# Optimization experiments

Hardware: AMD Instinct MI355X
Metric: run time of the kernel (lower is better)

The kernel has to match this reference:

```python
import jax, jax.numpy as jnp
import numpy as np

N = 8192        # agents (single node type VEHICLE)
K = 15          # max_Nnode - 1 neighbors per node
E = N * K       # edges
FT = 12         # prediction horizon steps
SD = 4          # state dim (x, y, vx, vy)
ID = 2          # input dim (ax, ay)
ZD = 8          # latent z dim
HE = 256        # history_enc_dim
EE = 128        # edge_enc_dim
OH = 256        # obs_lstm_hidden_dim
GH = 256        # guide_RNN_hidden_dim
FH = 256        # FC_hidden_dim
AD = 16         # att_internal_dim
DT = 0.25
SCALE = 1.0     # input_scale


def setup_inputs() -> dict:
    ks = jax.random.split(jax.random.key(0), 40)
    f = lambda i, s: jax.random.normal(ks[i], s, jnp.float32)
    w = lambda i, s: 0.05 * jax.random.normal(ks[i], s, jnp.float32)
    inp = dict(
        x_last=f(0, (N, SD)), x_st_last=f(1, (N, SD)), hist_enc=f(2, (N, HE)),
        z=f(3, (N, ZD)),
        node_size=jax.random.uniform(ks[4], (N, 2), jnp.float32, 1.0, 3.0),
        W_h0=w(5, (SD, OH)), b_h0=w(6, (OH,)), W_c0=w(7, (SD, OH)), b_c0=w(8, (OH,)),
        W_gh=w(9, (HE + ZD, GH)), b_gh=w(10, (GH,)),
        W_gru_ih=w(11, (HE + ZD, 3 * GH)), W_gru_hh=w(12, (GH, 3 * GH)),
        b_gru_ih=w(13, (3 * GH,)), b_gru_hh=w(14, (3 * GH,)),
        W_proj=w(15, (GH, 2)), b_proj=w(16, (2,)),
        W_att1=w(17, (EE, AD)), W_att2=w(18, (SD, AD)), v_att=w(19, (AD,)),
        W_lstm_ih=w(20, (EE, 4 * OH)), W_lstm_hh=w(21, (OH, 4 * OH)),
        b_lstm_ih=w(22, (4 * OH,)), b_lstm_hh=w(23, (4 * OH,)),
        W_e1=w(24, (SD + 4, FH)), b_e1=w(25, (FH,)), W_e2=w(26, (FH, EE)), b_e2=w(27, (EE,)),
        W_a1=w(28, (OH + ZD + SD + 4, FH)), b_a1=w(29, (FH,)),
        W_a2=w(30, (FH, ID)), b_a2=w(31, (ID,)),
    )
    # edge k is the j-th neighbor of node k // K; index 0 in the enc table is the pad row
    inp["edge_idx1"] = jnp.repeat(jnp.arange(N), K)
    inp["edge_idx2"] = jax.random.randint(ks[32], (E,), 0, N)
    inp["node_obs_idx"] = (jnp.arange(E) + 1).reshape(N, K)
    inp["ft"] = FT
    return inp


def _dyn(s, u):
    # double-integrator: s = [x, y, vx, vy], u = [ax, ay]
    pos = s[:, :2] + s[:, 2:4] * DT + 0.5 * u * DT * DT
    vel = s[:, 2:4] + u * DT
    return jnp.concatenate([pos, vel], -1)


def _forward(x_last, x_st_last, hist_enc, z, node_size,
             W_h0, b_h0, W_c0, b_c0, W_gh, b_gh, W_gru_ih, W_gru_hh, b_gru_ih, b_gru_hh,
             W_proj, b_proj, W_att1, W_att2, v_att, W_lstm_ih, W_lstm_hh, b_lstm_ih, b_lstm_hh,
             W_e1, b_e1, W_e2, b_e2, W_a1, b_a1, W_a2, b_a2,
             edge_idx1, edge_idx2, node_obs_idx, ft):
    n = x_last.shape[0]
    ee = W_e2.shape[1]
    # ---- guide GRU: desired trajectory [ft, N, 2] ----
    xz = jnp.concatenate([hist_enc, z], -1)
    h0g = xz @ W_gh + b_gh
    gi = xz @ W_gru_ih + b_gru_ih  # input is constant over time (xz repeated)
    ir, iz, inn = jnp.split(gi, 3, -1)

    def gru_step(h, _):
        hr, hz, hn = jnp.split(h @ W_gru_hh + b_gru_hh, 3, -1)
        r = jax.nn.sigmoid(ir + hr)
        u = jax.nn.sigmoid(iz + hz)
        nh = (1.0 - u) * jnp.tanh(inn + r * hn) + u * h
        return nh, nh

    _, hs = jax.lax.scan(gru_step, h0g, None, length=ft)
    des = hs @ W_proj + b_proj                       # [ft, N, 2]
    des_next = jnp.concatenate([des[1:], des[-1:]], 0)
    des_prev = jnp.concatenate([jnp.zeros_like(des[:1]), des[:-1]], 0)
    first = jnp.zeros((ft,), jnp.float32).at[0].set(1.0)

    # ---- obs LSTM initial state ----
    h0 = x_st_last @ W_h0 + b_h0
    c0 = x_st_last @ W_c0 + b_c0

    size1 = node_size[edge_idx1]
    size2 = node_size[edge_idx2]
    rad = 0.5 * (jnp.linalg.norm(size1, axis=-1) + jnp.linalg.norm(size2, axis=-1))

    def step(carry, xs):
        prev, prev_st, h, c, terr, ccost = carry
        des_t, des_n, des_p, fst = xs
        # edge gather + collision cost + edge encoding
        s1 = prev[edge_idx1]
        s2 = prev[edge_idx2]
        dist = jnp.linalg.norm(s1[:, :2] - s2[:, :2], axis=-1)
        ccost = ccost + jnp.sum(jax.nn.relu(rad - dist))
        feat = jnp.concatenate([s2 - s1, size1, size2], -1)          # [E, SD+4]
        enc = jax.nn.relu(feat @ W_e1 + b_e1) @ W_e2 + b_e2          # [E, EE]
        enc_all = jnp.concatenate([jnp.zeros((1, ee), enc.dtype), enc], 0)
        obs = enc_all[node_obs_idx]                                   # [N, K, EE]
        # relative state (t==0 uses standardized history directly)
        m = 1.0 - fst
        rel = prev_st - m * x_st_last
        rel = jnp.concatenate([rel[:, :2] - m * des_p, rel[:, 2:]], -1)
        terr = terr + jnp.linalg.norm(rel[:, :2]) / n
        next_wp = des_t - prev_st[:, :2]
        next_wp2 = des_n - prev_st[:, :2]
        # additive attention over neighbors
        scores = jnp.tanh(obs @ W_att1 + (rel @ W_att2)[:, None, :]) @ v_att   # [N, K]
        att = jax.nn.softmax(scores, axis=-1)
        ctx = jnp.einsum('nk,nkd->nd', att, obs)
        # LSTM cell (torch gate order i, f, g, o)
        gates = ctx @ W_lstm_ih + b_lstm_ih + h @ W_lstm_hh + b_lstm_hh
        g_i, g_f, g_g, g_o = jnp.split(gates, 4, -1)
        c = jax.nn.sigmoid(g_f) * c + jax.nn.sigmoid(g_i) * jnp.tanh(g_g)
        h = jax.nn.sigmoid(g_o) * jnp.tanh(c)
        # action net + dynamics rollout
        a_in = jnp.concatenate([h, z, rel, next_wp, next_wp2], -1)   # [N, OH+ZD+SD+4]
        u = SCALE * jnp.tanh(jax.nn.relu(a_in @ W_a1 + b_a1) @ W_a2 + b_a2)
        nxt = _dyn(prev, u)
        nxt_st = _dyn(prev_st, u)
        return (nxt, nxt_st, h, c, terr, ccost), (nxt, u)

    zero = jnp.zeros((), jnp.float32)
    init = (x_last, x_st_last, h0, c0, zero, zero)
    (_, _, _, _, terr, ccost), (state_pred, input_pred) = jax.lax.scan(
        step, init, (des, des_next, des_prev, first))
    return state_pred, input_pred, terr, ccost


def reference(x_last, x_st_last, hist_enc, z, node_size,
              W_h0, b_h0, W_c0, b_c0, W_gh, b_gh, W_gru_ih, W_gru_hh, b_gru_ih, b_gru_hh,
              W_proj, b_proj, W_att1, W_att2, v_att, W_lstm_ih, W_lstm_hh, b_lstm_ih, b_lstm_hh,
              W_e1, b_e1, W_e2, b_e2, W_a1, b_a1, W_a2, b_a2,
              edge_idx1, edge_idx2, node_obs_idx, ft):
    return _forward(x_last, x_st_last, hist_enc, z, node_size,
                    W_h0, b_h0, W_c0, b_c0, W_gh, b_gh, W_gru_ih, W_gru_hh, b_gru_ih, b_gru_hh,
                    W_proj, b_proj, W_att1, W_att2, v_att, W_lstm_ih, W_lstm_hh, b_lstm_ih, b_lstm_hh,
                    W_e1, b_e1, W_e2, b_e2, W_a1, b_a1, W_a2, b_a2,
                    edge_idx1, edge_idx2, node_obs_idx, ft)
```

## Files before the change

### kernel.cpp

```cpp
#include <hip/hip_runtime.h>

#define DEVI __device__ __forceinline__

constexpr int N_  = 8192;
constexpr int K_  = 15;
constexpr int E_  = N_ * K_;
constexpr int FTS = 12;
constexpr float DT_ = 0.25f;

typedef __attribute__((ext_vector_type(8))) short short8x;
typedef __attribute__((ext_vector_type(4))) float float4x;

union U8 { unsigned int u[4]; short8x v; };

DEVI float sigf(float x) { return 1.0f / (1.0f + __expf(-x)); }
DEVI float tanhf_fast(float x) { float e = __expf(2.f * x); return 1.f - 2.f / (e + 1.f); }
DEVI unsigned int f2u(float x) { union { float f; unsigned int u; } c; c.f = x; return c.u; }
DEVI float u2f(unsigned int x) { union { unsigned int u; float f; } c; c.u = x; return c.f; }

DEVI void split8(const float* __restrict__ s, short8x& hi8, short8x& lo8) {
  U8 ph, pl;
#pragma unroll
  for (int p = 0; p < 4; p++) {
    float a0 = s[2*p], a1 = s[2*p+1];
    unsigned int u0 = f2u(a0), u1 = f2u(a1);
    unsigned int h0 = u0 & 0xFFFF0000u, h1 = u1 & 0xFFFF0000u;
    ph.u[p] = (u0 >> 16) | h1;
    float l0 = a0 - u2f(h0), l1 = a1 - u2f(h1);
    pl.u[p] = (f2u(l0) >> 16) | (f2u(l1) & 0xFFFF0000u);
  }
  hi8 = ph.v; lo8 = pl.v;
}

__global__ void k_zero(float* ss) {
  ss[blockIdx.x * 256 + threadIdx.x] = 0.f;
}

__global__ __launch_bounds__(256) void k_init_des(const float* __restrict__ b_proj,
                                                  float* __restrict__ des) {
  int i = blockIdx.x * 256 + threadIdx.x;
  des[i*2]     = b_proj[0];
  des[i*2 + 1] = b_proj[1];
}

__global__ __launch_bounds__(256) void k_edge_static(
    const int* __restrict__ e1, const int* __restrict__ e2,
    const float* __restrict__ nsize, float* __restrict__ rad, float* __restrict__ szf)
{
  int e = blockIdx.x * 256 + threadIdx.x;
  if (e >= E_) return;
  int i1 = e1[e], i2 = e2[e];
  float s1x = nsize[i1*2+0], s1y = nsize[i1*2+1];
  float s2x = nsize[i2*2+0], s2y = nsize[i2*2+1];
  rad[e] = 0.5f * (sqrtf(s1x*s1x + s1y*s1y) + sqrtf(s2x*s2x + s2y*s2y));
  *(float4*)&szf[e*4] = make_float4(s1x, s1y, s2x, s2y);
}

__global__ __launch_bounds__(256) void k_prep_hi(
    const float* __restrict__ W, unsigned short* __restrict__ out)
{
  int t = blockIdx.x * 256 + threadIdx.x;
  int fid = t >> 6, L = t & 63;
  int ks = fid >> 3, nt = fid & 7;
  int k0 = ks * 32 + (L >> 4) * 8;
  int n  = nt * 16 + (L & 15);
  unsigned int hi[4];
#pragma unroll
  for (int p = 0; p < 4; p++) {
    float w0 = W[(size_t)(k0 + 2*p) * 128 + n];
    float w1 = W[(size_t)(k0 + 2*p + 1) * 128 + n];
    hi[p] = (f2u(w0) >> 16) | (f2u(w1) & 0xFFFF0000u);
  }
  *(uint4*)(out + (size_t)fid * 512 + (size_t)L * 8) = make_uint4(hi[0], hi[1], hi[2], hi[3]);
}

__global__ __launch_bounds__(256) void k_prep1(
    const float* __restrict__ WA, const float* __restrict__ WB,
    int mode, int split, int wA, int wB, int Ktot, int NT, int nfrag,
    unsigned short* __restrict__ out)
{
  int t = blockIdx.x * 256 + threadIdx.x;
  int fid = t >> 6, L = t & 63;
  if (fid >= nfrag) return;
  int ks = fid / NT, nt = fid % NT;
  int k0 = ks * 32 + (L >> 4) * 8;
  int n  = nt * 16 + (L & 15);
  unsigned int hi[4];
#pragma unroll
  for (int p = 0; p < 4; p++) {
    float w0 = 0.f, w1 = 0.f;
    int ka = k0 + 2*p, kb = ka + 1;
    if (mode == 0) {
      if (ka < Ktot) w0 = (ka < split) ? WA[(size_t)ka*wA + n] : WB[(size_t)(ka-split)*wB + n];
      if (kb < Ktot) w1 = (kb < split) ? WA[(size_t)kb*wA + n] : WB[(size_t)(kb-split)*wB + n];
    } else {
      if (ka < Ktot) w0 = (n < split) ? WA[(size_t)ka*wA + n] : WB[(size_t)ka*wB + (n-split)];
      if (kb < Ktot) w1 = (n < split) ? WA[(size_t)kb*wA + n] : WB[(size_t)kb*wB + (n-split)];
    }
    hi[p] = (f2u(w0) >> 16) | (f2u(w1) & 0xFFFF0000u);
  }
  *(uint4*)(out + (size_t)fid * 512 + (size_t)L * 8) = make_uint4(hi[0], hi[1], hi[2], hi[3]);
}

__global__ __launch_bounds__(256) void k_xz_mfma(
    const float* __restrict__ hist, const float* __restrict__ z,
    const unsigned short* __restrict__ wB,
    const float* __restrict__ b_gh, const float* __restrict__ b_gih,
    float* __restrict__ gh0, float* __restrict__ gi)
{
  __shared__ __align__(16) float Abuf[2][64][36];
  const int tid = threadIdx.x;
  const int w = tid >> 6, lane = tid & 63;
  const int m = lane & 15, q = lane >> 4;
  const int n0 = blockIdx.x * 64;
  const int r_ = tid >> 2, c_ = (tid & 3) * 8;
  float4x acc[16];
#pragma unroll
  for (int tl = 0; tl < 16; tl++) acc[tl] = (float4x){0.f,0.f,0.f,0.f};

  auto LD = [&](int ks, float4& v0, float4& v1) {
    int kk = ks*32 + c_;
    int n = n0 + r_;
    if (kk < 256) {
      v0 = *(const float4*)&hist[(size_t)n*256 + kk];
      v1 = *(const float4*)&hist[(size_t)n*256 + kk + 4];
    } else if (kk == 256) {
      v0 = *(const float4*)&z[n*8];
      v1 = *(const float4*)&z[n*8 + 4];
    } else {
      v0 = make_float4(0,0,0,0); v1 = v0;
    }
  };
  {
    float4 v0, v1; LD(0, v0, v1);
    *(float4*)&Abuf[0][r_][c_]     = v0;
    *(float4*)&Abuf[0][r_][c_ + 4] = v1;
  }
  __syncthreads();
  for (int ks = 0; ks < 9; ks++) {
    float4 v0, v1;
    if (ks < 8) LD(ks + 1, v0, v1);
    short8x aHi, aLo;
    split8(&Abuf[ks & 1][w*16 + m][q*8], aHi, aLo);
#pragma unroll
    for (int tl = 0; tl < 16; tl++) {
      int nt = blockIdx.y*16 + tl;
      size_t off = (size_t)(ks*64 + nt) * 512 + (size_t)lane*8;
      short8x bh = *(const short8x*)(wB + off);
      acc[tl] = __builtin_amdgcn_mfma_f32_16x16x32_bf16(aLo, bh, acc[tl], 0, 0, 0);
      acc[tl] = __builtin_amdgcn_mfma_f32_16x16x32_bf16(aHi, bh, acc[tl], 0, 0, 0);
    }
    if (ks < 8) {
      *(float4*)&Abuf[(ks+1) & 1][r_][c_]     = v0;
      *(float4*)&Abuf[(ks+1) & 1][r_][c_ + 4] = v1;
      __syncthreads();
    }
  }
#pragma unroll
  for (int tl = 0; tl < 16; tl++) {
    int col = (blockIdx.y*16 + tl)*16 + m;
    float bias = (col < 256) ? b_gh[col] : b_gih[col - 256];
#pragma unroll
    for (int i = 0; i < 4; i++) {
      int n = n0 + w*16 + q*4 + i;
      float v = acc[tl][i] + bias;
      if (col < 256) gh0[(size_t)n*256 + col] = v;
      else           gi[(size_t)n*768 + col - 256] = v;
    }
  }
}

DEVI void gru_core(float* sm, int tid, int n0, int j0,
                   const float* __restrict__ h_in, const unsigned short* __restrict__ wB,
                   const float* __restrict__ b_hh, const float* __restrict__ gi,
                   const float* __restrict__ W_proj, float* __restrict__ des_t,
                   float* __restrict__ h_out)
{
  float (*A0)[36] = (float (*)[36])sm;
  float (*A1)[36] = (float (*)[36])(sm + 2304);
  const int w = tid >> 6, lane = tid & 63;
  const int m = lane & 15, q = lane >> 4;
  const int r_ = tid >> 2, c_ = (tid & 3) * 8;
  float4x acc[12];
#pragma unroll
  for (int tl = 0; tl < 12; tl++) acc[tl] = (float4x){0.f,0.f,0.f,0.f};

  {
    float4 p0 = *(const float4*)&h_in[(size_t)(n0 + r_)*256 + c_];
    float4 p1 = *(const float4*)&h_in[(size_t)(n0 + r_)*256 + c_ + 4];
    *(float4*)&A0[r_][c_]     = p0;
    *(float4*)&A0[r_][c_ + 4] = p1;
  }
  __syncthreads();
  for (int ks = 0; ks < 8; ks++) {
    float4 p0, p1;
    if (ks < 7) {
      int kk = (ks + 1)*32 + c_;
      p0 = *(const float4*)&h_in[(size_t)(n0 + r_)*256 + kk];
      p1 = *(const float4*)&h_in[(size_t)(n0 + r_)*256 + kk + 4];
    }
    float (*Ac)[36] = (ks & 1) ? A1 : A0;
    short8x aHi, aLo;
    split8(&Ac[w*16 + m][q*8], aHi, aLo);
#pragma unroll
    for (int tl = 0; tl < 12; tl++) {
      int g = tl >> 2, jt = tl & 3;
      int nt = g*16 + (j0 >> 4) + jt;
      size_t off = (size_t)(ks*48 + nt) * 512 + (size_t)lane*8;
      short8x bh = *(const short8x*)(wB + off);
      acc[tl] = __builtin_amdgcn_mfma_f32_16x16x32_bf16(aLo, bh, acc[tl], 0, 0, 0);
      acc[tl] = __builtin_amdgcn_mfma_f32_16x16x32_bf16(aHi, bh, acc[tl], 0, 0, 0);
    }
    if (ks < 7) {
      float (*An)[36] = (ks & 1) ? A0 : A1;
      *(float4*)&An[r_][c_]     = p0;
      *(float4*)&An[r_][c_ + 4] = p1;
      __syncthreads();
    }
  }
  float pd0[4] = {0,0,0,0}, pd1[4] = {0,0,0,0};
#pragma unroll
  for (int jt = 0; jt < 4; jt++) {
    int j = j0 + jt*16 + m;
    float br = b_hh[j], bz = b_hh[256 + j], bn = b_hh[512 + j];
    float wp0 = W_proj[j*2], wp1 = W_proj[j*2 + 1];
#pragma unroll
    for (int i = 0; i < 4; i++) {
      int n = n0 + w*16 + q*4 + i;
      float ir  = gi[(size_t)n*768 + j];
      float iz  = gi[(size_t)n*768 + 256 + j];
      float inn = gi[(size_t)n*768 + 512 + j];
      float hold = h_in[(size_t)n*256 + j];
      float r = sigf(ir + acc[0*4 + jt][i] + br);
      float u = sigf(iz + acc[1*4 + jt][i] + bz);
      float nh = (1.f - u) * tanhf_fast(inn + r * (acc[2*4 + jt][i] + bn)) + u * hold;
      h_out[(size_t)n*256 + j] = nh;
      pd0[i] += nh * wp0;
      pd1[i] += nh * wp1;
    }
  }
#pragma unroll
  for (int off = 1; off < 16; off <<= 1) {
#pragma unroll
    for (int i = 0; i < 4; i++) {
      pd0[i] += __shfl_xor(pd0[i], off);
      pd1[i] += __shfl_xor(pd1[i], off);
    }
  }
  if (m == 0) {
#pragma unroll
    for (int i = 0; i < 4; i++) {
      int n = n0 + w*16 + q*4 + i;
      atomicAdd(&des_t[n*2],     pd0[i]);
      atomicAdd(&des_t[n*2 + 1], pd1[i]);
    }
  }
}

__global__ __launch_bounds__(256) void k_gru_mfma(
    const float* __restrict__ h_in, const unsigned short* __restrict__ wB,
    const float* __restrict__ b_hh, const float* __restrict__ gi,
    const float* __restrict__ W_proj, float* __restrict__ des_t,
    float* __restrict__ h_out)
{
  __shared__ __align__(16) float smem[4608];
  gru_core(smem, threadIdx.x, blockIdx.x * 64, blockIdx.y * 64,
           h_in, wB, b_hh, gi, W_proj, des_t, h_out);
}

__global__ __launch_bounds__(256) void k_lstm_mfma(
    const float* __restrict__ ctxg, const float* __restrict__ h_in,
    const unsigned short* __restrict__ wB,
    const float* __restrict__ b_ih, const float* __restrict__ b_hh,
    float* __restrict__ c_st, float* __restrict__ h_out)
{
  __shared__ __align__(16) float Abuf[2][64][36];
  const int tid = threadIdx.x;
  const int w = tid >> 6, lane = tid & 63;
  const int m = lane & 15, q = lane >> 4;
  const int n0 = blockIdx.x * 64;
  const int j0 = blockIdx.y * 32;
  const int r_ = tid >> 2, c_ = (tid & 3) * 8;
  float4x acc[8];
#pragma unroll
  for (int tl = 0; tl < 8; tl++) acc[tl] = (float4x){0.f,0.f,0.f,0.f};

  auto LD = [&](int ks, float4& v0, float4& v1) {
    int kk = ks*32 + c_;
    int n = n0 + r_;
    if (kk < 128) {
      v0 = *(const float4*)&ctxg[(size_t)n*128 + kk];
      v1 = *(const float4*)&ctxg[(size_t)n*128 + kk + 4];
    } else {
      v0 = *(const float4*)&h_in[(size_t)n*256 + kk - 128];
      v1 = *(const float4*)&h_in[(size_t)n*256 + kk - 124];
    }
  };
  {
    float4 v0, v1; LD(0, v0, v1);
    *(float4*)&Abuf[0][r_][c_]     = v0;
    *(float4*)&Abuf[0][r_][c_ + 4] = v1;
  }
  __syncthreads();
  for (int ks = 0; ks < 12; ks++) {
    float4 v0, v1;
    if (ks < 11) LD(ks + 1, v0, v1);
    short8x aHi, aLo;
    split8(&Abuf[ks & 1][w*16 + m][q*8], aHi, aLo);
#pragma unroll
    for (int tl = 0; tl < 8; tl++) {
      int g = tl >> 1, jt = tl & 1;
      int nt = g*16 + (j0 >> 4) + jt;
      size_t off = (size_t)(ks*64 + nt) * 512 + (size_t)lane*8;
      short8x bh = *(const short8x*)(wB + off);
      acc[tl] = __builtin_amdgcn_mfma_f32_16x16x32_bf16(aLo, bh, acc[tl], 0, 0, 0);
      acc[tl] = __builtin_amdgcn_mfma_f32_16x16x32_bf16(aHi, bh, acc[tl], 0, 0, 0);
    }
    if (ks < 11) {
      *(float4*)&Abuf[(ks+1) & 1][r_][c_]     = v0;
      *(float4*)&Abuf[(ks+1) & 1][r_][c_ + 4] = v1;
      __syncthreads();
    }
  }
#pragma unroll
  for (int jt = 0; jt < 2; jt++) {
    int j = j0 + jt*16 + m;
    float bi = b_ih[j]       + b_hh[j];
    float bf = b_ih[256 + j] + b_hh[256 + j];
    float bg = b_ih[512 + j] + b_hh[512 + j];
    float bo = b_ih[768 + j] + b_hh[768 + j];
#pragma unroll
    for (int i = 0; i < 4; i++) {
      int n = n0 + w*16 + q*4 + i;
      float g_i = sigf(acc[0*2 + jt][i] + bi);
      float g_f = sigf(acc[1*2 + jt][i] + bf);
      float g_g = tanhf_fast(acc[2*2 + jt][i] + bg);
      float g_o = sigf(acc[3*2 + jt][i] + bo);
      float cv = g_f * c_st[(size_t)n*256 + j] + g_i * g_g;
      c_st[(size_t)n*256 + j] = cv;
      h_out[(size_t)n*256 + j] = g_o * tanhf_fast(cv);
    }
  }
}

__global__ __launch_bounds__(256) void k_action_mfma(
    const float* __restrict__ h, const float* __restrict__ z,
    const float* __restrict__ rel, const float* __restrict__ nwp, const float* __restrict__ nwp2,
    const unsigned short* __restrict__ wB, const float* __restrict__ b_a1,
    const float* __restrict__ W_a2, const float* __restrict__ b_a2,
    float* __restrict__ prev, float* __restrict__ prev_st,
    float* __restrict__ outS, float* __restrict__ outU)
{
  __shared__ __align__(16) float Abuf[2][32][36];
  __shared__ float sm_p[2][16][2];
  const int tid = threadIdx.x;
  const int w = tid >> 6, lane = tid & 63;
  const int m = lane & 15, q = lane >> 4;
  const int ng = w >> 1, hh = w & 1;
  const int n0 = blockIdx.x * 32;
  const int r_ = tid >> 3, c_ = (tid & 7) * 4;
  float4x acc[8];
#pragma unroll
  for (int j = 0; j < 8; j++) acc[j] = (float4x){0.f,0.f,0.f,0.f};

  auto LD = [&](int ks) -> float4 {
    int kk = ks*32 + c_;
    int n = n0 + r_;
    float4 v;
    if (kk < 256)       v = *(const float4*)&h[(size_t)n*256 + kk];
    else if (kk == 256) v = *(const float4*)&z[n*8];
    else if (kk == 260) v = *(const float4*)&z[n*8 + 4];
    else if (kk == 264) v = *(const float4*)&rel[n*4];
    else if (kk == 268) {
      float2 w1 = *(const float2*)&nwp[n*2];
      float2 w2 = *(const float2*)&nwp2[n*2];
      v = make_float4(w1.x, w1.y, w2.x, w2.y);
    } else v = make_float4(0,0,0,0);
    return v;
  };
  {
    float4 v = LD(0);
    *(float4*)&Abuf[0][r_][c_] = v;
  }
  __syncthreads();
  for (int ks = 0; ks < 9; ks++) {
    float4 v;
    if (ks < 8) v = LD(ks + 1);
    short8x aHi, aLo;
    split8(&Abuf[ks & 1][ng*16 + m][q*8], aHi, aLo);
#pragma unroll
    for (int j = 0; j < 8; j++) {
      int tl = hh*8 + j;
      size_t off = (size_t)(ks*16 + tl) * 512 + (size_t)lane*8;
      short8x bh = *(const short8x*)(wB + off);
      acc[j] = __builtin_amdgcn_mfma_f32_16x16x32_bf16(aLo, bh, acc[j], 0, 0, 0);
      acc[j] = __builtin_amdgcn_mfma_f32_16x16x32_bf16(aHi, bh, acc[j], 0, 0, 0);
    }
    if (ks < 8) {
      *(float4*)&Abuf[(ks+1) & 1][r_][c_] = v;
      __syncthreads();
    }
  }
  float p0[4] = {0,0,0,0}, p1[4] = {0,0,0,0};
#pragma unroll
  for (int j = 0; j < 8; j++) {
    int col = (hh*8 + j)*16 + m;
    float ba = b_a1[col];
    float2 w2 = *(const float2*)&W_a2[col*2];
#pragma unroll
    for (int i = 0; i < 4; i++) {
      float hv = fmaxf(acc[j][i] + ba, 0.f);
      p0[i] += hv * w2.x;
      p1[i] += hv * w2.y;
    }
  }
#pragma unroll
  for (int off = 1; off < 16; off <<= 1) {
#pragma unroll
    for (int i = 0; i < 4; i++) {
      p0[i] += __shfl_xor(p0[i], off);
      p1[i] += __shfl_xor(p1[i], off);
    }
  }
  if (hh == 1 && m == 0) {
#pragma unroll
    for (int i = 0; i < 4; i++) {
      sm_p[ng][q*4 + i][0] = p0[i];
      sm_p[ng][q*4 + i][1] = p1[i];
    }
  }
  __syncthreads();
  if (hh == 0 && m == 0) {
    float ba0 = b_a2[0], ba1 = b_a2[1];
    const float hd = 0.5f * DT_ * DT_;
#pragma unroll
    for (int i = 0; i < 4; i++) {
      int n = n0 + ng*16 + q*4 + i;
      float ux = tanhf_fast(p0[i] + sm_p[ng][q*4 + i][0] + ba0);
      float uy = tanhf_fast(p1[i] + sm_p[ng][q*4 + i][1] + ba1);
      float4 pv = *(const float4*)&prev[n*4];
      float4 ps = *(const float4*)&prev_st[n*4];
      float4 npv, nps;
      npv.x = pv.x + pv.z*DT_ + ux*hd;
      npv.y = pv.y + pv.w*DT_ + uy*hd;
      npv.z = pv.z + ux*DT_;
      npv.w = pv.w + uy*DT_;
      nps.x = ps.x + ps.z*DT_ + ux*hd;
      nps.y = ps.y + ps.w*DT_ + uy*hd;
      nps.z = ps.z + ux*DT_;
      nps.w = ps.w + uy*DT_;
      *(float4*)&prev[n*4] = npv;
      *(float4*)&prev_st[n*4] = nps;
      *(float4*)&outS[(size_t)n*4] = npv;
      outU[n*2]     = ux;
      outU[n*2 + 1] = uy;
    }
  }
}

__global__ __launch_bounds__(256) void k_init_hc(
    const float* __restrict__ x_last, const float* __restrict__ x_st_last,
    const float* __restrict__ W_h0, const float* __restrict__ b_h0,
    const float* __restrict__ W_c0, const float* __restrict__ b_c0,
    float* __restrict__ h, float* __restrict__ c,
    float* __restrict__ prev, float* __restrict__ prev_st)
{
  const int n = blockIdx.x;
  const int j = threadIdx.x;
  float x0 = x_st_last[n*4], x1 = x_st_last[n*4+1], x2 = x_st_last[n*4+2], x3 = x_st_last[n*4+3];
  h[(size_t)n*256 + j] = b_h0[j] + x0*W_h0[j] + x1*W_h0[256+j] + x2*W_h0[512+j] + x3*W_h0[768+j];
  c[(size_t)n*256 + j] = b_c0[j] + x0*W_c0[j] + x1*W_c0[256+j] + x2*W_c0[512+j] + x3*W_c0[768+j];
  if (j < 4) prev[n*4 + j] = x_last[n*4 + j];
  else if (j < 8) prev_st[n*4 + (j-4)] = x_st_last[n*4 + (j-4)];
}

__global__ __launch_bounds__(256, 4) void k_edge_gru(
    const float* __restrict__ prev, const float* __restrict__ prev_st,
    const float* __restrict__ x_st_last,
    const float* __restrict__ szf, const float* __restrict__ rad,
    const int* __restrict__ nobs, const int* __restrict__ e1, const int* __restrict__ e2,
    const float* __restrict__ W_e1, const float* __restrict__ b_e1,
    const unsigned short* __restrict__ wsB, const float* __restrict__ b_e2,
    const unsigned short* __restrict__ wattA, const float* __restrict__ W_att2,
    const float* __restrict__ v_att,
    const float* __restrict__ des_p, const float* __restrict__ des_t,
    const float* __restrict__ des_n,
    float* __restrict__ relg, float* __restrict__ nwp, float* __restrict__ nwp2,
    float* __restrict__ ctx, float* __restrict__ ss_t, float* __restrict__ cc,
    const float* __restrict__ g_hin, const unsigned short* __restrict__ wBg,
    const float* __restrict__ b_ghh, const float* __restrict__ gi,
    const float* __restrict__ W_proj, float* __restrict__ des_g,
    float* __restrict__ g_hout, int gru_on)
{
  __shared__ __align__(16) float smem[4776];
  const int tid = threadIdx.x;
  const int bid = blockIdx.x;

  if ((bid % 5) == 4) {
    if (!gru_on) return;
    int b = bid / 5;
    gru_core(smem, tid, (b & 127) * 64, (b >> 7) * 64,
             g_hin, wBg, b_ghh, gi, W_proj, des_g, g_hout);
    return;
  }
  const int eb = bid - (bid + 1) / 5;

  float* sm_stage = smem;
  float* sm_feats = smem + 4096;
  float* sm_flags = smem + 4608;
  float* sm_relv  = smem + 4672;
  float* sm_watt2 = smem + 4688;
  float* sm_vatt  = smem + 4752;
  float* sm_red   = smem + 4768;

  const int n0  = eb * 4;
  const int slot = (eb & 15) << 4;
  const int lane = tid & 63;
  const int g    = tid >> 6;
  const int q = lane >> 4, m = lane & 15;

  if (tid >= 176 && tid < 192) sm_vatt[tid - 176] = v_att[tid - 176];
  if (tid >= 192) sm_watt2[tid - 192] = W_att2[tid - 192];

  if (tid < 64) {
    float v = 0.f;
    if (tid < 60) {
      int gg = tid / 15, k = tid % 15;
      int idx = nobs[(n0 + gg) * 15 + k];
      float f[8] = {0,0,0,0,0,0,0,0};
      float fl = 0.f;
      if (idx > 0) {
        int e = idx - 1;
        int i1 = e1[e], i2 = e2[e];
#pragma unroll
        for (int d = 0; d < 4; d++) f[d] = prev[i2*4 + d] - prev[i1*4 + d];
        float4 sz = *(const float4*)&szf[(size_t)e*4];
        f[4] = sz.x; f[5] = sz.y; f[6] = sz.z; f[7] = sz.w;
        fl = 1.f;
        float dist = sqrtf(f[0]*f[0] + f[1]*f[1]);
        v = fmaxf(rad[e] - dist, 0.f);
      }
#pragma unroll
      for (int d = 0; d < 8; d++) sm_feats[(gg*16 + k)*8 + d] = f[d];
      sm_flags[gg*16 + k] = fl;
    } else {
      int gg = tid - 60;
#pragma unroll
      for (int d = 0; d < 8; d++) sm_feats[(gg*16 + 15)*8 + d] = 0.f;
      sm_flags[gg*16 + 15] = 0.f;
    }
#pragma unroll
    for (int off = 32; off; off >>= 1) v += __shfl_down(v, off);
    if (tid == 0) atomicAdd(cc + slot, v);
  } else if (tid < 68) {
    int gg = tid - 64;
    int n = n0 + gg;
    float4 ps = *(const float4*)&prev_st[n*4];
    float r0, r1, r2, r3;
    if (des_p) {
      float4 xs = *(const float4*)&x_st_last[n*4];
      r0 = ps.x - xs.x - des_p[n*2];
      r1 = ps.y - xs.y - des_p[n*2 + 1];
      r2 = ps.z - xs.z;
      r3 = ps.w - xs.w;
    } else { r0 = ps.x; r1 = ps.y; r2 = ps.z; r3 = ps.w; }
    sm_relv[gg*4+0] = r0; sm_relv[gg*4+1] = r1; sm_relv[gg*4+2] = r2; sm_relv[gg*4+3] = r3;
    *(float4*)&relg[n*4] = make_float4(r0, r1, r2, r3);
    nwp[n*2]      = des_t[n*2]     - ps.x;
    nwp[n*2 + 1]  = des_t[n*2 + 1] - ps.y;
    nwp2[n*2]     = des_n[n*2]     - ps.x;
    nwp2[n*2 + 1] = des_n[n*2 + 1] - ps.y;
    sm_red[gg] = r0*r0 + r1*r1;
  }
  {
    const uint4* src = (const uint4*)wsB;
    uint4* dst = (uint4*)sm_stage;
    dst[tid]       = src[tid];
    dst[tid + 256] = src[tid + 256];
  }
  __syncthreads();
  if (tid == 64) atomicAdd(ss_t + slot, sm_red[0] + sm_red[1] + sm_red[2] + sm_red[3]);

  float f[8];
  {
    const float4 fa = *(const float4*)&sm_feats[(g*16 + m)*8];
    const float4 fb = *(const float4*)&sm_feats[(g*16 + m)*8 + 4];
    f[0]=fa.x; f[1]=fa.y; f[2]=fa.z; f[3]=fa.w; f[4]=fb.x; f[5]=fb.y; f[6]=fb.z; f[7]=fb.w;
  }
  float4x encR[8];
#pragma unroll
  for (int nt = 0; nt < 8; nt++) encR[nt] = (float4x){0.f,0.f,0.f,0.f};
  const float4* We14 = (const float4*)W_e1;
  const float4* Be14 = (const float4*)b_e1;

  for (int ks = 0; ks < 8; ks++) {
    uint4 r0, r1;
    if (ks < 7) {
      const uint4* src = (const uint4*)wsB + (ks + 1) * 512;
      r0 = src[tid];
      r1 = src[tid + 256];
    }
    short8x aHi, aLo;
    {
      float h8[8];
      float4 b0 = Be14[8*ks + 2*q];
      float4 b1 = Be14[8*ks + 2*q + 1];
      h8[0]=b0.x; h8[1]=b0.y; h8[2]=b0.z; h8[3]=b0.w; h8[4]=b1.x; h8[5]=b1.y; h8[6]=b1.z; h8[7]=b1.w;
#pragma unroll
      for (int d = 0; d < 8; d++) {
        float4 wa = We14[d*64 + ks*8 + 2*q];
        float4 wb = We14[d*64 + ks*8 + 2*q + 1];
        h8[0] += f[d]*wa.x; h8[1] += f[d]*wa.y; h8[2] += f[d]*wa.z; h8[3] += f[d]*wa.w;
        h8[4] += f[d]*wb.x; h8[5] += f[d]*wb.y; h8[6] += f[d]*wb.z; h8[7] += f[d]*wb.w;
      }
#pragma unroll
      for (int p = 0; p < 8; p++) h8[p] = fmaxf(h8[p], 0.f);
      split8(h8, aHi, aLo);
    }
    const unsigned short* sb = (const unsigned short*)sm_stage + (ks & 1) * 4096;
#pragma unroll
    for (int nt = 0; nt < 8; nt++) {
      short8x bh = *(const short8x*)(sb + nt*512 + lane*8);
      encR[nt] = __builtin_amdgcn_mfma_f32_16x16x32_bf16(aLo, bh, encR[nt], 0, 0, 0);
      encR[nt] = __builtin_amdgcn_mfma_f32_16x16x32_bf16(aHi, bh, encR[nt], 0, 0, 0);
    }
    if (ks < 7) {
      uint4* dst = (uint4*)sm_stage + ((ks + 1) & 1) * 512;
      dst[tid]       = r0;
      dst[tid + 256] = r1;
      __syncthreads();
    }
  }
  float4x fl4 = *(const float4x*)&sm_flags[g*16 + q*4];
#pragma unroll
  for (int nt = 0; nt < 8; nt++) {
    float b2 = b_e2[nt*16 + m];
#pragma unroll
    for (int i = 0; i < 4; i++) encR[nt][i] = (encR[nt][i] + b2) * fl4[i];
  }

  __syncthreads();
  {
  }
  float* tb = sm_stage + g * 576;
  float4x sacc = {0.f, 0.f, 0.f, 0.f};
#pragma unroll
  for (int ksc = 0; ksc < 4; ksc++) {
#pragma unroll
    for (int ntl = 0; ntl < 2; ntl++) {
#pragma unroll
      for (int i = 0; i < 4; i++)
        tb[(q*4 + i)*36 + ntl*16 + m] = encR[2*ksc + ntl][i];
    }
    __builtin_amdgcn_s_waitcnt(0);
    float a8[8];
    {
      const float4* tp = (const float4*)(tb + m*36 + q*8);
      float4 t0 = tp[0], t1 = tp[1];
      a8[0]=t0.x; a8[1]=t0.y; a8[2]=t0.z; a8[3]=t0.w;
      a8[4]=t1.x; a8[5]=t1.y; a8[6]=t1.z; a8[7]=t1.w;
    }
    __builtin_amdgcn_s_waitcnt(0);
    short8x aH, aL;
    split8(a8, aH, aL);
    short8x bh = *(const short8x*)(wattA + ksc*512 + lane*8);
    sacc = __builtin_amdgcn_mfma_f32_16x16x32_bf16(aL, bh, sacc, 0, 0, 0);
    sacc = __builtin_amdgcn_mfma_f32_16x16x32_bf16(aH, bh, sacc, 0, 0, 0);
  }

  float relw;
  {
    float4 rv = *(const float4*)&sm_relv[g*4];
    relw = rv.x * sm_watt2[m] + rv.y * sm_watt2[16 + m]
         + rv.z * sm_watt2[32 + m] + rv.w * sm_watt2[48 + m];
  }
  float vat = sm_vatt[m];
  float val[4];
#pragma unroll
  for (int i = 0; i < 4; i++) val[i] = tanhf_fast(sacc[i] + relw) * vat;
#pragma unroll
  for (int msk = 1; msk < 16; msk <<= 1) {
#pragma unroll
    for (int i = 0; i < 4; i++) val[i] += __shfl_xor(val[i], msk);
  }
  if (q == 3) val[3] = -3.0e38f;
  float mx = fmaxf(fmaxf(val[0], val[1]), fmaxf(val[2], val[3]));
  mx = fmaxf(mx, __shfl_xor(mx, 16));
  mx = fmaxf(mx, __shfl_xor(mx, 32));
  float4x ev;
  float ssum = 0.f;
#pragma unroll
  for (int i = 0; i < 4; i++) { ev[i] = __expf(val[i] - mx); ssum += ev[i]; }
  ssum += __shfl_xor(ssum, 16);
  ssum += __shfl_xor(ssum, 32);
  float inv = 1.f / ssum;
#pragma unroll
  for (int i = 0; i < 4; i++) ev[i] *= inv;

  float cpart[8];
#pragma unroll
  for (int nt = 0; nt < 8; nt++) {
    float cv = ev[0]*encR[nt][0] + ev[1]*encR[nt][1] + ev[2]*encR[nt][2] + ev[3]*encR[nt][3];
    cv += __shfl_xor(cv, 16);
    cv += __shfl_xor(cv, 32);
    cpart[nt] = cv;
  }
  float v0 = (q == 0) ? cpart[0] : (q == 1) ? cpart[2] : (q == 2) ? cpart[4] : cpart[6];
  float v1 = (q == 0) ? cpart[1] : (q == 1) ? cpart[3] : (q == 2) ? cpart[5] : cpart[7];
  size_t cb = (size_t)(n0 + g) * 128 + q*32 + m;
  ctx[cb]      = v0;
  ctx[cb + 16] = v1;
}

__global__ void k_final(const float* __restrict__ ss, float* __restrict__ out) {
  const int lane = threadIdx.x;
  float red[13];
#pragma unroll
  for (int a = 0; a < 13; a++) {
    float v = (lane < 16) ? ss[a*256 + lane*16] : 0.f;
    v += __shfl_xor(v, 1);
    v += __shfl_xor(v, 2);
    v += __shfl_xor(v, 4);
    v += __shfl_xor(v, 8);
    red[a] = v;
  }
  if (lane == 0) {
    float t = 0.f;
    for (int i = 0; i < FTS; i++) t += sqrtf(red[i]);
    out[(size_t)FTS * N_ * 6]     = t / (float)N_;
    out[(size_t)FTS * N_ * 6 + 1] = red[12];
  }
}

extern "C" void kernel_launch(void* const* d_in, const int* in_sizes, int n_in,
                              void* d_out, int out_size, void* d_ws, size_t ws_size,
                              hipStream_t stream) {
  (void)in_sizes; (void)n_in; (void)out_size;
  const float* x_last    = (const float*)d_in[0];
  const float* x_st_last = (const float*)d_in[1];
  const float* hist_enc  = (const float*)d_in[2];
  const float* z         = (const float*)d_in[3];
  const float* node_size = (const float*)d_in[4];
  const float* W_h0 = (const float*)d_in[5];
  const float* b_h0 = (const float*)d_in[6];
  const float* W_c0 = (const float*)d_in[7];
  const float* b_c0 = (const float*)d_in[8];
  const float* W_gh = (const float*)d_in[9];
  const float* b_gh = (const float*)d_in[10];
  const float* W_gih = (const float*)d_in[11];
  const float* W_ghh = (const float*)d_in[12];
  const float* b_gih = (const float*)d_in[13];
  const float* b_ghh = (const float*)d_in[14];
  const float* W_proj = (const float*)d_in[15];
  const float* b_proj = (const float*)d_in[16];
  const float* W_att1 = (const float*)d_in[17];
  const float* W_att2 = (const float*)d_in[18];
  const float* v_att  = (const float*)d_in[19];
  const float* W_lih = (const float*)d_in[20];
  const float* W_lhh = (const float*)d_in[21];
  const float* b_lih = (const float*)d_in[22];
  const float* b_lhh = (const float*)d_in[23];
  const float* W_e1 = (const float*)d_in[24];
  const float* b_e1 = (const float*)d_in[25];
  const float* W_e2 = (const float*)d_in[26];
  const float* b_e2 = (const float*)d_in[27];
  const float* W_a1 = (const float*)d_in[28];
  const float* b_a1 = (const float*)d_in[29];
  const float* W_a2 = (const float*)d_in[30];
  const float* b_a2 = (const float*)d_in[31];
  const int* e1   = (const int*)d_in[32];
  const int* e2   = (const int*)d_in[33];
  const int* nobs = (const int*)d_in[34];
  float* out = (float*)d_out;

  float* wsf     = (float*)d_ws;
  float* prev    = wsf;
  float* prev_st = wsf + 32768;
  float* des     = wsf + 65536;
  float* rad     = wsf + 262160;
  float* szf     = wsf + 385040;
  float* baseA   = wsf + 876560;
  float* gh0 = baseA;
  float* gh1 = baseA + (size_t)N_ * 256;
  float* gi  = baseA + (size_t)2 * N_ * 256;
  float* hA   = baseA;
  float* hB   = baseA + (size_t)N_ * 256;
  float* cbuf = baseA + (size_t)2 * N_ * 256;
  float* ctx  = baseA + (size_t)3 * N_ * 256;
  float* rel  = baseA + (size_t)4 * N_ * 256;
  float* nwp  = rel + (size_t)N_ * 4;
  float* nwp2 = nwp + (size_t)N_ * 2;
  unsigned short* wsBe = (unsigned short*)(wsf + 11362320);
  unsigned short* wsBg = (unsigned short*)(wsf + 11427856);
  unsigned short* wsBl = (unsigned short*)(wsf + 11624464);
  unsigned short* wsBx = (unsigned short*)(wsf + 12017680);
  unsigned short* wsBa = (unsigned short*)(wsf + 12312592);
  unsigned short* wattA = (unsigned short*)(wsf + 12386320);
  float* ssx = wsf + 12388368;
  float* ext = wsf + 12391696;
  const size_t needF = 12391696ull + 5ull * N_ * 256ull;
  const bool fuse = ws_size >= needF * 4ull;
  float* gh0F = fuse ? ext : gh0;
  float* gh1F = fuse ? (ext + (size_t)N_ * 256) : gh1;
  float* giF  = fuse ? (ext + (size_t)2 * N_ * 256) : gi;

  k_zero<<<13, 256, 0, stream>>>(ssx);
  k_edge_static<<<(E_ + 255) / 256, 256, 0, stream>>>(e1, e2, node_size, rad, szf);
  k_init_des<<<FTS * N_ / 256, 256, 0, stream>>>(b_proj, des);

  k_prep_hi<<<16, 256, 0, stream>>>(W_e2, wsBe);
  k_prep1<<<96,  256, 0, stream>>>(W_ghh, W_ghh, 0, 256, 768,  768,  256, 48, 384, wsBg);
  k_prep1<<<192, 256, 0, stream>>>(W_lih, W_lhh, 0, 128, 1024, 1024, 384, 64, 768, wsBl);
  k_prep1<<<144, 256, 0, stream>>>(W_gh,  W_gih, 1, 256, 256,  768,  264, 64, 576, wsBx);
  k_prep1<<<36,  256, 0, stream>>>(W_a1,  W_a1,  0, 272, 256,  256,  272, 16, 144, wsBa);
  k_prep1<<<1,   256, 0, stream>>>(W_att1, W_att1, 0, 128, 16, 16, 128, 1, 4, wattA);

  k_xz_mfma<<<dim3(128, 4), 256, 0, stream>>>(hist_enc, z, wsBx, b_gh, b_gih, gh0F, giF);
  const int pre = fuse ? 2 : FTS;
  float* gcur = gh0F;
  float* gnxt = gh1F;
  for (int t = 0; t < pre; t++) {
    k_gru_mfma<<<dim3(128, 4), 256, 0, stream>>>(gcur, wsBg, b_ghh, giF, W_proj,
                                                 des + (size_t)t * N_ * 2, gnxt);
    float* tmp = gcur; gcur = gnxt; gnxt = tmp;
  }

  k_init_hc<<<N_, 256, 0, stream>>>(x_last, x_st_last, W_h0, b_h0, W_c0, b_c0,
                                    hA, cbuf, prev, prev_st);
  float* hcur = hA;
  float* hnxt = hB;
  for (int t = 0; t < FTS; t++) {
    const float* des_t = des + (size_t)t * N_ * 2;
    const float* des_n = des + (size_t)((t + 1 < FTS) ? t + 1 : FTS - 1) * N_ * 2;
    const float* des_p = (t > 0) ? des + (size_t)(t - 1) * N_ * 2 : nullptr;
    const int gs = t + 2;
    const int gru_on = (fuse && gs < FTS) ? 1 : 0;
    const float* gin = (gs & 1) ? gh1F : gh0F;
    float* gout      = (gs & 1) ? gh0F : gh1F;
    float* des_g = des + (size_t)((gs < FTS) ? gs : 0) * N_ * 2;
    k_edge_gru<<<2560, 256, 0, stream>>>(prev, prev_st, x_st_last, szf, rad,
                                         nobs, e1, e2, W_e1, b_e1, wsBe, b_e2,
                                         wattA, W_att2, v_att,
                                         des_p, des_t, des_n,
                                         rel, nwp, nwp2, ctx,
                                         ssx + (size_t)t * 256, ssx + 12 * 256,
                                         gin, wsBg, b_ghh, giF, W_proj, des_g, gout, gru_on);
    k_lstm_mfma<<<dim3(128, 8), 256, 0, stream>>>(ctx, hcur, wsBl, b_lih, b_lhh,
                                                  cbuf, hnxt);
    k_action_mfma<<<256, 256, 0, stream>>>(hnxt, z, rel, nwp, nwp2,
                                           wsBa, b_a1, W_a2, b_a2,
                                           prev, prev_st,
                                           out + (size_t)t * N_ * 4,
                                           out + (size_t)FTS * N_ * 4 + (size_t)t * N_ * 2);
    float* tmp = hcur; hcur = hnxt; hnxt = tmp;
  }
  k_final<<<1, 64, 0, stream>>>(ssx, out);
}
```

Baseline: 1.503 ms.

## Halve GRU tile rows and split waves across row/column halves

The GRU MFMA core now processes 32 rows per block instead of 64, with the four waves split into two row halves times two column halves, so each wave holds 6 accumulators instead of 12. This doubles the GRU block count and changes the interleaving in the fused edge+GRU kernel from 4:1 to 2:1 edge-to-GRU blocks, giving a 3072-block grid. The aim is to cut per-block register and LDS footprint and spread GRU work more finely across CUs alongside the edge work. The trade-off is that the B-weight fragments are reloaded by twice as many blocks, which raises total weight traffic.

```diff
diff --git a/kernel.cpp b/kernel.cpp
--- a/kernel.cpp
+++ b/kernel.cpp
@@ -177,63 +177,59 @@
                    float* __restrict__ h_out)
 {
   float (*A0)[36] = (float (*)[36])sm;
-  float (*A1)[36] = (float (*)[36])(sm + 2304);
+  float (*A1)[36] = (float (*)[36])(sm + 1152);
   const int w = tid >> 6, lane = tid & 63;
   const int m = lane & 15, q = lane >> 4;
-  const int r_ = tid >> 2, c_ = (tid & 3) * 8;
-  float4x acc[12];
-#pragma unroll
-  for (int tl = 0; tl < 12; tl++) acc[tl] = (float4x){0.f,0.f,0.f,0.f};
+  const int rh = w & 1, jh = w >> 1;
+  const int r_ = tid >> 3, c_ = (tid & 7) * 4;
+  float4x acc[6];
+#pragma unroll
+  for (int t6 = 0; t6 < 6; t6++) acc[t6] = (float4x){0.f,0.f,0.f,0.f};
 
   {
-    float4 p0 = *(const float4*)&h_in[(size_t)(n0 + r_)*256 + c_];
-    float4 p1 = *(const float4*)&h_in[(size_t)(n0 + r_)*256 + c_ + 4];
-    *(float4*)&A0[r_][c_]     = p0;
-    *(float4*)&A0[r_][c_ + 4] = p1;
+    float4 p = *(const float4*)&h_in[(size_t)(n0 + r_)*256 + c_];
+    *(float4*)&A0[r_][c_] = p;
   }
   __syncthreads();
   for (int ks = 0; ks < 8; ks++) {
-    float4 p0, p1;
+    float4 p;
     if (ks < 7) {
-      int kk = (ks + 1)*32 + c_;
-      p0 = *(const float4*)&h_in[(size_t)(n0 + r_)*256 + kk];
-      p1 = *(const float4*)&h_in[(size_t)(n0 + r_)*256 + kk + 4];
+      p = *(const float4*)&h_in[(size_t)(n0 + r_)*256 + (ks + 1)*32 + c_];
     }
     float (*Ac)[36] = (ks & 1) ? A1 : A0;
     short8x aHi, aLo;
-    split8(&Ac[w*16 + m][q*8], aHi, aLo);
-#pragma unroll
-    for (int tl = 0; tl < 12; tl++) {
-      int g = tl >> 2, jt = tl & 3;
-      int nt = g*16 + (j0 >> 4) + jt;
+    split8(&Ac[rh*16 + m][q*8], aHi, aLo);
+#pragma unroll
+    for (int t6 = 0; t6 < 6; t6++) {
+      int g = t6 >> 1, jj = t6 & 1;
+      int nt = g*16 + (j0 >> 4) + jh*2 + jj;
       size_t off = (size_t)(ks*48 + nt) * 512 + (size_t)lane*8;
       short8x bh = *(const short8x*)(wB + off);
-      acc[tl] = __builtin_amdgcn_mfma_f32_16x16x32_bf16(aLo, bh, acc[tl], 0, 0, 0);
-      acc[tl] = __builtin_amdgcn_mfma_f32_16x16x32_bf16(aHi, bh, acc[tl], 0, 0, 0);
+      acc[t6] = __builtin_amdgcn_mfma_f32_16x16x32_bf16(aLo, bh, acc[t6], 0, 0, 0);
+      acc[t6] = __builtin_amdgcn_mfma_f32_16x16x32_bf16(aHi, bh, acc[t6], 0, 0, 0);
     }
     if (ks < 7) {
       float (*An)[36] = (ks & 1) ? A0 : A1;
-      *(float4*)&An[r_][c_]     = p0;
-      *(float4*)&An[r_][c_ + 4] = p1;
+      *(float4*)&An[r_][c_] = p;
       __syncthreads();
     }
   }
   float pd0[4] = {0,0,0,0}, pd1[4] = {0,0,0,0};
 #pragma unroll
-  for (int jt = 0; jt < 4; jt++) {
-    int j = j0 + jt*16 + m;
+  for (int jj = 0; jj < 2; jj++) {
+    int j = j0 + (jh*2 + jj)*16 + m;
     float br = b_hh[j], bz = b_hh[256 + j], bn = b_hh[512 + j];
     float wp0 = W_proj[j*2], wp1 = W_proj[j*2 + 1];
 #pragma unroll
     for (int i = 0; i < 4; i++) {
-      int n = n0 + w*16 + q*4 + i;
+      int n = n0 + rh*16 + q*4 + i;
       float ir  = gi[(size_t)n*768 + j];
       float iz  = gi[(size_t)n*768 + 256 + j];
       float inn = gi[(size_t)n*768 + 512 + j];
       float hold = h_in[(size_t)n*256 + j];
-      float r = sigf(ir + acc[0*4 + jt][i] + br);
-      float u = sigf(iz + acc[1*4 + jt][i] + bz);
-      float nh = (1.f - u) * tanhf_fast(inn + r * (acc[2*4 + jt][i] + bn)) + u * hold;
+      float r = sigf(ir + acc[0*2 + jj][i] + br);
+      float u = sigf(iz + acc[1*2 + jj][i] + bz);
+      float nh = (1.f - u) * tanhf_fast(inn + r * (acc[2*2 + jj][i] + bn)) + u * hold;
       h_out[(size_t)n*256 + j] = nh;
       pd0[i] += nh * wp0;
       pd1[i] += nh * wp1;
@@ -250,7 +246,7 @@
   if (m == 0) {
 #pragma unroll
     for (int i = 0; i < 4; i++) {
-      int n = n0 + w*16 + q*4 + i;
+      int n = n0 + rh*16 + q*4 + i;
       atomicAdd(&des_t[n*2],     pd0[i]);
       atomicAdd(&des_t[n*2 + 1], pd1[i]);
     }
@@ -263,8 +259,8 @@
     const float* __restrict__ W_proj, float* __restrict__ des_t,
     float* __restrict__ h_out)
 {
-  __shared__ __align__(16) float smem[4608];
-  gru_core(smem, threadIdx.x, blockIdx.x * 64, blockIdx.y * 64,
+  __shared__ __align__(16) float smem[2304];
+  gru_core(smem, threadIdx.x, blockIdx.x * 32, blockIdx.y * 64,
            h_in, wB, b_hh, gi, W_proj, des_t, h_out);
 }
 
@@ -495,15 +491,16 @@
   __shared__ __align__(16) float smem[4776];
   const int tid = threadIdx.x;
   const int bid = blockIdx.x;
-
-  if ((bid % 5) == 4) {
+  const int third = bid / 3, rem = bid - third * 3;
+
+  if (rem == 2) {
     if (!gru_on) return;
-    int b = bid / 5;
-    gru_core(smem, tid, (b & 127) * 64, (b >> 7) * 64,
+    int b = third;
+    gru_core(smem, tid, (b & 255) * 32, (b >> 8) * 64,
              g_hin, wBg, b_ghh, gi, W_proj, des_g, g_hout);
     return;
   }
-  const int eb = bid - (bid + 1) / 5;
+  const int eb = third * 2 + rem;
 
   float* sm_stage = smem;
   float* sm_feats = smem + 4096;
@@ -820,7 +817,7 @@
   float* gcur = gh0F;
   float* gnxt = gh1F;
   for (int t = 0; t < pre; t++) {
-    k_gru_mfma<<<dim3(128, 4), 256, 0, stream>>>(gcur, wsBg, b_ghh, giF, W_proj,
+    k_gru_mfma<<<dim3(256, 4), 256, 0, stream>>>(gcur, wsBg, b_ghh, giF, W_proj,
                                                  des + (size_t)t * N_ * 2, gnxt);
     float* tmp = gcur; gcur = gnxt; gnxt = tmp;
   }
@@ -838,7 +835,7 @@
     const float* gin = (gs & 1) ? gh1F : gh0F;
     float* gout      = (gs & 1) ? gh0F : gh1F;
     float* des_g = des + (size_t)((gs < FTS) ? gs : 0) * N_ * 2;
-    k_edge_gru<<<2560, 256, 0, stream>>>(prev, prev_st, x_st_last, szf, rad,
+    k_edge_gru<<<3072, 256, 0, stream>>>(prev, prev_st, x_st_last, szf, rad,
                                          nobs, e1, e2, W_e1, b_e1, wsBe, b_e2,
                                          wattA, W_att2, v_att,
                                          des_p, des_t, des_n,
```

Result: slower. 1.670 ms (+11.1%).
